# Kernel tuning notes

Hardware: AMD Instinct MI355X
Metric: run time of the kernel (lower is better)

The kernel has to match this reference:

```python
import jax, jax.numpy as jnp
import numpy as np

LN_EPS = 1e-5


def _layernorm(h, gamma, beta):
    mu = jnp.mean(h, axis=-1, keepdims=True)
    var = jnp.mean(jnp.square(h - mu), axis=-1, keepdims=True)
    return (h - mu) * jax.lax.rsqrt(var + LN_EPS) * gamma + beta


def setup_inputs() -> dict:
    key = jax.random.key(0)
    ks = jax.random.split(key, 8)
    B, D, d_model, vocab = 8, 14, 256, 1024
    n_leaf = 2 ** D
    leaf_ids = jax.random.randint(ks[0], (B, n_leaf), 0, vocab)
    op_ids = jax.random.randint(ks[1], (B, n_leaf - 1), 0, vocab)  # heap/BFS order
    tok_emb = jax.random.normal(ks[2], (vocab, d_model), jnp.float32)
    dep_emb = jax.random.normal(ks[3], (15, d_model), jnp.float32)
    idx_emb = jax.random.normal(ks[4], (2, d_model), jnp.float32)
    W = jax.random.normal(ks[5], (7 * d_model, d_model), jnp.float32) / np.sqrt(7 * d_model)
    b = jnp.zeros((d_model,), jnp.float32)
    gamma = jnp.ones((d_model,), jnp.float32)
    beta = jnp.zeros((d_model,), jnp.float32)
    return {"leaf_ids": leaf_ids, "op_ids": op_ids, "tok_emb": tok_emb,
            "dep_emb": dep_emb, "idx_emb": idx_emb, "W": W, "b": b,
            "gamma": gamma, "beta": beta}


def reference(leaf_ids, op_ids, tok_emb, dep_emb, idx_emb, W, b, gamma, beta):
    B, n_leaf = leaf_ids.shape
    D = int(np.log2(n_leaf))  # leaf depth
    d_model = tok_emb.shape[1]
    # leaves: token embedding + depth embedding (OpCombiner path for non-Op nodes)
    emb = tok_emb[leaf_ids] + dep_emb[D]                       # [B, 2^D, dm]
    # process internal levels bottom-up (fixed-size loop over tree depth)
    for d in reversed(range(D)):
        n = 2 ** d
        nid = op_ids[:, n - 1:2 * n - 1]                       # [B, n]
        left, right = emb[:, 0::2], emb[:, 1::2]              # children depth d+1
        e_op = tok_emb[nid]                                    # [B, n, dm]
        dvec = jnp.broadcast_to(dep_emb[d + 1], (B, n, d_model))
        il = jnp.broadcast_to(idx_emb[0], (B, n, d_model))
        ir = jnp.broadcast_to(idx_emb[1], (B, n, d_model))
        x = jnp.concatenate([e_op, left, right, dvec, il, dvec, ir], axis=-1)  # [B,n,7dm]
        h = jax.nn.relu(jnp.einsum('bnk,kd->bnd', x, W) + b)
        emb = _layernorm(h, gamma, beta)
    return emb[:, 0]                                           # root embedding [B, dm]
```

## Files before the change

### kernel.cpp

```cpp
#include <hip/hip_runtime.h>

typedef float f32x4 __attribute__((ext_vector_type(4)));
typedef short bf16x8 __attribute__((ext_vector_type(8)));

__device__ inline unsigned short f2bf(float f) {
    unsigned int u = __builtin_bit_cast(unsigned int, f);
    unsigned int r = (u + 0x7FFFu + ((u >> 16) & 1u)) >> 16;
    return (unsigned short)r;
}
__device__ inline float bf2f(unsigned short u) {
    unsigned int x = ((unsigned int)u) << 16;
    return __builtin_bit_cast(float, x);
}
__device__ inline float f4get(const float4& v, int e) {
    return e == 0 ? v.x : (e == 1 ? v.y : (e == 2 ? v.z : v.w));
}

__global__ __launch_bounds__(256) void k_prep(const float* __restrict__ tok,
                                              const float* __restrict__ W,
                                              const float* __restrict__ dep,
                                              const float* __restrict__ idx,
                                              const float* __restrict__ bvec,
                                              unsigned short* __restrict__ tokbf,
                                              unsigned short* __restrict__ WTbf,
                                              float* __restrict__ carrp) {
    __shared__ float s_tile[64][65];
    int bx = blockIdx.x;
    if (bx < 256) {
        int i = bx * 256 + threadIdx.x;
        const float4 v = *(const float4*)(tok + (long)i * 4);
        ushort4 o;
        o.x = f2bf(v.x); o.y = f2bf(v.y); o.z = f2bf(v.z); o.w = f2bf(v.w);
        *(ushort4*)(tokbf + (long)i * 4) = o;
    } else if (bx < 304) {
        int bb = bx - 256;
        int sec = bb >> 4;
        int tt = bb & 15;
        int k0 = (tt >> 2) * 64, j0 = (tt & 3) * 64;
        int tx = threadIdx.x & 63, ty = threadIdx.x >> 6;
#pragma unroll
        for (int r = 0; r < 16; r++) {
            int kk = ty * 16 + r;
            s_tile[kk][tx] = W[(sec * 256 + k0 + kk) * 256 + j0 + tx];
        }
        __syncthreads();
#pragma unroll
        for (int r = 0; r < 16; r++) {
            int jj = ty * 16 + r;
            WTbf[(sec * 256 + j0 + jj) * 256 + k0 + tx] = f2bf(s_tile[tx][jj]);
        }
    } else {
        int q = bx - 304;
        int d = q >> 3;
        int c = q & 7;
        int j = threadIdx.x;
        float acc = (c == 0) ? bvec[j] : 0.f;
        int kbeg = c * 32, kend = kbeg + 32;
#pragma unroll 4
        for (int k = kbeg; k < kend; k++) {
            float dv = dep[(d + 1) * 256 + k];
            acc += dv * (W[(768 + k) * 256 + j] + W[(1280 + k) * 256 + j]);
            acc += idx[k] * W[(1024 + k) * 256 + j];
            acc += idx[256 + k] * W[(1536 + k) * 256 + j];
        }
        if (d == 13) {
#pragma unroll 4
            for (int k = kbeg; k < kend; k++) {
                float dv = dep[14 * 256 + k];
                acc += dv * (W[(256 + k) * 256 + j] + W[(512 + k) * 256 + j]);
            }
        }
        carrp[(long)q * 256 + j] = acc;
    }
}

__global__ __launch_bounds__(256) void k_carrsum(const float* __restrict__ carrp,
                                                 float* __restrict__ carr) {
    int d = blockIdx.x;
    int j = threadIdx.x;
    float s = 0.f;
#pragma unroll
    for (int c = 0; c < 8; c++) s += carrp[(long)(d * 8 + c) * 256 + j];
    carr[d * 256 + j] = s;
}

__global__ __launch_bounds__(256) void k_ttmm(const unsigned short* __restrict__ tokbf,
                                              const unsigned short* __restrict__ WTbf,
                                              unsigned short* __restrict__ T) {
    int wid = threadIdx.x >> 6, lane = threadIdx.x & 63;
    int l15 = lane & 15, l4 = lane >> 4;
    int row0 = blockIdx.x * 32;
    int sec = blockIdx.y;

    f32x4 acc[2][4] = {};
    for (int kk = 0; kk < 8; kk++) {
        int k0 = kk * 32 + l4 * 8;
        bf16x8 af[2], bfr[4];
#pragma unroll
        for (int mi = 0; mi < 2; mi++)
            af[mi] = *(const bf16x8*)(tokbf + (long)(row0 + mi * 16 + l15) * 256 + k0);
#pragma unroll
        for (int ni = 0; ni < 4; ni++)
            bfr[ni] = *(const bf16x8*)(WTbf + (long)(sec * 256 + wid * 64 + ni * 16 + l15) * 256 + k0);
#pragma unroll
        for (int mi = 0; mi < 2; mi++)
#pragma unroll
            for (int ni = 0; ni < 4; ni++)
                acc[mi][ni] = __builtin_amdgcn_mfma_f32_16x16x32_bf16(af[mi], bfr[ni],
                                                                     acc[mi][ni], 0, 0, 0);
    }
#pragma unroll
    for (int mi = 0; mi < 2; mi++)
#pragma unroll
        for (int r = 0; r < 4; r++) {
            int row = row0 + mi * 16 + l4 * 4 + r;
#pragma unroll
            for (int ni = 0; ni < 4; ni++) {
                int c = wid * 64 + ni * 16 + l15;
                T[(long)sec * 262144 + (long)row * 256 + c] = f2bf(acc[mi][ni][r]);
            }
        }
}

__global__ __launch_bounds__(256) void k_level12f(const int* __restrict__ leaf_ids,
                                                  const int* __restrict__ op_ids,
                                                  const unsigned short* __restrict__ T,
                                                  const float* __restrict__ carr,
                                                  const float* __restrict__ gamma,
                                                  const float* __restrict__ beta,
                                                  const unsigned short* __restrict__ WTbf,
                                                  unsigned short* __restrict__ ebuf_out) {
    __shared__ unsigned short sA[64 * 256];
    __shared__ int s_nid13[64];
    __shared__ int s_leaf[128];
    __shared__ int s_nid[32];
    __shared__ float s_part[4][32][2];
    int b = blockIdx.y;
    int row0 = blockIdx.x * 32;
    int t = threadIdx.x;
    int wid = t >> 6, lane = t & 63;
    int l15 = lane & 15, l4 = lane >> 4;
    const unsigned short* T0 = T;
    const unsigned short* T1 = T + 262144;
    const unsigned short* T2 = T + 524288;

    if (t < 64) s_nid13[t] = op_ids[b * 16383 + 8191 + 2 * row0 + t];
    if (t < 128) s_leaf[t] = leaf_ids[b * 16384 + 4 * row0 + t];
    if (t < 32) s_nid[t] = op_ids[b * 16383 + 4095 + row0 + t];
    __syncthreads();

    {
        const float* c13 = carr + 13 * 256;
        float4 dd[4], g4[4], b4[4];
#pragma unroll
        for (int q = 0; q < 4; q++) {
            int c0 = l15 * 16 + q * 4;
            dd[q] = *(const float4*)(c13 + c0);
            g4[q] = *(const float4*)(gamma + c0);
            b4[q] = *(const float4*)(beta + c0);
        }
#pragma unroll
        for (int j = 0; j < 4; j++) {
            int node = wid * 16 + j * 4 + l4;
            int nid = s_nid13[node];
            int ll = s_leaf[2 * node], lr = s_leaf[2 * node + 1];
            bf16x8 a0 = *(const bf16x8*)(T0 + (long)nid * 256 + l15 * 16);
            bf16x8 a1 = *(const bf16x8*)(T0 + (long)nid * 256 + l15 * 16 + 8);
            bf16x8 b0 = *(const bf16x8*)(T1 + (long)ll * 256 + l15 * 16);
            bf16x8 b1 = *(const bf16x8*)(T1 + (long)ll * 256 + l15 * 16 + 8);
            bf16x8 c0 = *(const bf16x8*)(T2 + (long)lr * 256 + l15 * 16);
            bf16x8 c1 = *(const bf16x8*)(T2 + (long)lr * 256 + l15 * 16 + 8);
            float v[16];
            float s = 0.f, s2 = 0.f;
#pragma unroll
            for (int e = 0; e < 8; e++) {
                float x = bf2f((unsigned short)a0[e]) + bf2f((unsigned short)b0[e]) +
                          bf2f((unsigned short)c0[e]) + f4get(dd[e >> 2], e & 3);
                x = fmaxf(x, 0.f);
                v[e] = x;
                s += x;
                s2 += x * x;
            }
#pragma unroll
            for (int e = 0; e < 8; e++) {
                float x = bf2f((unsigned short)a1[e]) + bf2f((unsigned short)b1[e]) +
                          bf2f((unsigned short)c1[e]) + f4get(dd[2 + (e >> 2)], e & 3);
                x = fmaxf(x, 0.f);
                v[8 + e] = x;
                s += x;
                s2 += x * x;
            }
#pragma unroll
            for (int m = 1; m < 16; m <<= 1) {
                s += __shfl_xor(s, m);
                s2 += __shfl_xor(s2, m);
            }
            float mu = s * (1.f / 256.f);
            float rs = rsqrtf(s2 * (1.f / 256.f) - mu * mu + 1e-5f);
            int swz = ((node >> 1) & 7) << 4;
            bf16x8 o0, o1;
#pragma unroll
            for (int e = 0; e < 8; e++) {
                o0[e] = (short)f2bf((v[e] - mu) * rs * f4get(g4[e >> 2], e & 3) +
                                    f4get(b4[e >> 2], e & 3));
                o1[e] = (short)f2bf((v[8 + e] - mu) * rs * f4get(g4[2 + (e >> 2)], e & 3) +
                                    f4get(b4[2 + (e >> 2)], e & 3));
            }
            *(bf16x8*)((char*)sA + node * 512 + ((l15 * 32) ^ swz)) = o0;
            *(bf16x8*)((char*)sA + node * 512 + ((l15 * 32 + 16) ^ swz)) = o1;
        }
    }
    __syncthreads();

    f32x4 acc[2][4] = {};
    for (int kk = 0; kk < 16; kk++) {
        int k0 = kk * 32 + l4 * 8;
        int hi = k0 >> 8;
        int binr = (k0 & 255) * 2;
        bf16x8 af[2], bfr[4];
#pragma unroll
        for (int mi = 0; mi < 2; mi++) {
            int node = 2 * (mi * 16 + l15) + hi;
            af[mi] = *(const bf16x8*)((const char*)sA + node * 512 + (binr ^ (((node >> 1) & 7) << 4)));
        }
        const unsigned short* Wb = WTbf + (long)(256 + hi * 256) * 256;
        int innerk = k0 & 255;
#pragma unroll
        for (int ni = 0; ni < 4; ni++) {
            int cn = wid * 64 + ni * 16 + l15;
            bfr[ni] = *(const bf16x8*)(Wb + (long)cn * 256 + innerk);
        }
#pragma unroll
        for (int mi = 0; mi < 2; mi++)
#pragma unroll
            for (int ni = 0; ni < 4; ni++)
                acc[mi][ni] = __builtin_amdgcn_mfma_f32_16x16x32_bf16(af[mi], bfr[ni],
                                                                     acc[mi][ni], 0, 0, 0);
    }

    const float* carr_d = carr + 12 * 256;
    float cv[4], gv[4], bv[4];
#pragma unroll
    for (int ni = 0; ni < 4; ni++) {
        int c = wid * 64 + ni * 16 + l15;
        cv[ni] = carr_d[c];
        gv[ni] = gamma[c];
        bv[ni] = beta[c];
    }

#pragma unroll
    for (int mi = 0; mi < 2; mi++) {
#pragma unroll
        for (int r = 0; r < 4; r++) {
            int row = mi * 16 + l4 * 4 + r;
            int nid = s_nid[row];
            float s = 0.f, s2 = 0.f;
#pragma unroll
            for (int ni = 0; ni < 4; ni++) {
                int c = wid * 64 + ni * 16 + l15;
                float h = acc[mi][ni][r] + bf2f(T0[(long)nid * 256 + c]) + cv[ni];
                h = fmaxf(h, 0.f);
                acc[mi][ni][r] = h;
                s += h;
                s2 += h * h;
            }
#pragma unroll
            for (int m = 1; m < 16; m <<= 1) {
                s += __shfl_xor(s, m);
                s2 += __shfl_xor(s2, m);
            }
            if (l15 == 0) {
                s_part[wid][row][0] = s;
                s_part[wid][row][1] = s2;
            }
        }
    }
    __syncthreads();

#pragma unroll
    for (int mi = 0; mi < 2; mi++) {
#pragma unroll
        for (int r = 0; r < 4; r++) {
            int row = mi * 16 + l4 * 4 + r;
            float s = s_part[0][row][0] + s_part[1][row][0] + s_part[2][row][0] + s_part[3][row][0];
            float s2 = s_part[0][row][1] + s_part[1][row][1] + s_part[2][row][1] + s_part[3][row][1];
            float mu = s * (1.f / 256.f);
            float rs = rsqrtf(s2 * (1.f / 256.f) - mu * mu + 1e-5f);
            unsigned short* o = ebuf_out + ((long)b * 4096 + row0 + row) * 256;
#pragma unroll
            for (int ni = 0; ni < 4; ni++) {
                int c = wid * 64 + ni * 16 + l15;
                o[c] = f2bf((acc[mi][ni][r] - mu) * rs * gv[ni] + bv[ni]);
            }
        }
    }
}

__global__ __attribute__((amdgpu_waves_per_eu(2, 2))) __launch_bounds__(512)
void k_mid(const unsigned short* __restrict__ prev,
           unsigned short* __restrict__ outbuf,
           const int* __restrict__ op_ids,
           const unsigned short* __restrict__ T0,
           const float* __restrict__ carr,
           const float* __restrict__ gamma,
           const float* __restrict__ beta,
           const unsigned short* __restrict__ WTbf) {
    __shared__ unsigned short sA[64 * 256];
    __shared__ unsigned short sB[64 * 256];
    __shared__ float s_part[8][64][2];
    int b = blockIdx.x >> 5;
    int q = blockIdx.x & 31;
    int t = threadIdx.x;
    int wid = t >> 6, lane = t & 63;
    int l15 = lane & 15, l4 = lane >> 4;

    bf16x8 breg[16][2];
#pragma unroll
    for (int kk = 0; kk < 16; kk++) {
        int k0 = kk * 32 + l4 * 8;
        int hi = k0 >> 8;
        int innerk = k0 & 255;
        const unsigned short* Wb = WTbf + (long)(256 + hi * 256) * 256;
#pragma unroll
        for (int ni = 0; ni < 2; ni++) {
            int cn = wid * 32 + ni * 16 + l15;
            breg[kk][ni] = *(const bf16x8*)(Wb + (long)cn * 256 + innerk);
        }
    }

    float gv[2], bv[2];
#pragma unroll
    for (int ni = 0; ni < 2; ni++) {
        int c = wid * 32 + ni * 16 + l15;
        gv[ni] = gamma[c];
        bv[ni] = beta[c];
    }

    unsigned short* cur = sA;
    unsigned short* nxt = sB;

    for (int ld = 11; ld >= 8; ld--) {
        int ng = 1 << ld;
        int m = ng >> 5;
        int mtiles = (m + 15) >> 4;

        float tv[4][4][2];
#pragma unroll
        for (int mi = 0; mi < 4; mi++)
            if (mi < mtiles)
#pragma unroll
                for (int r = 0; r < 4; r++) {
                    int row = mi * 16 + l4 * 4 + r;
                    int rc = row < m ? row : m - 1;
                    int nid = op_ids[b * 16383 + (ng - 1) + q * m + rc];
#pragma unroll
                    for (int ni = 0; ni < 2; ni++)
                        tv[mi][r][ni] = bf2f(T0[(long)nid * 256 + wid * 32 + ni * 16 + l15]);
                }

        f32x4 acc[4][2] = {};
        if (ld == 11) {
            const unsigned short* X = prev + ((long)b * 4096 + q * 128) * 256;
#pragma unroll
            for (int kk = 0; kk < 16; kk++) {
                int k0 = kk * 32 + l4 * 8;
                bf16x8 af[4];
#pragma unroll
                for (int mi = 0; mi < 4; mi++)
                    af[mi] = *(const bf16x8*)(X + (long)(mi * 16 + l15) * 512 + k0);
#pragma unroll
                for (int mi = 0; mi < 4; mi++)
#pragma unroll
                    for (int ni = 0; ni < 2; ni++)
                        acc[mi][ni] = __builtin_amdgcn_mfma_f32_16x16x32_bf16(af[mi], breg[kk][ni],
                                                                             acc[mi][ni], 0, 0, 0);
            }
        } else {
#pragma unroll
            for (int kk = 0; kk < 16; kk++) {
                int k0 = kk * 32 + l4 * 8;
                int hi = k0 >> 8;
                int binr = (k0 & 255) * 2;
                bf16x8 af[4];
#pragma unroll
                for (int mi = 0; mi < 4; mi++)
                    if (mi < mtiles) {
                        int node = 2 * (mi * 16 + l15) + hi;
                        af[mi] = *(const bf16x8*)((const char*)cur + node * 512 +
                                                  (binr ^ (((node >> 1) & 7) << 4)));
                    }
#pragma unroll
                for (int mi = 0; mi < 4; mi++)
                    if (mi < mtiles)
#pragma unroll
                        for (int ni = 0; ni < 2; ni++)
                            acc[mi][ni] = __builtin_amdgcn_mfma_f32_16x16x32_bf16(
                                af[mi], breg[kk][ni], acc[mi][ni], 0, 0, 0);
            }
        }

        const float* carr_d = carr + ld * 256;
        float cv[2];
#pragma unroll
        for (int ni = 0; ni < 2; ni++) cv[ni] = carr_d[wid * 32 + ni * 16 + l15];

#pragma unroll
        for (int mi = 0; mi < 4; mi++)
            if (mi < mtiles)
#pragma unroll
                for (int r = 0; r < 4; r++) {
                    float s = 0.f, s2 = 0.f;
#pragma unroll
                    for (int ni = 0; ni < 2; ni++) {
                        float hh = fmaxf(acc[mi][ni][r] + tv[mi][r][ni] + cv[ni], 0.f);
                        acc[mi][ni][r] = hh;
                        s += hh;
                        s2 += hh * hh;
                    }
#pragma unroll
                    for (int m2 = 1; m2 < 16; m2 <<= 1) {
                        s += __shfl_xor(s, m2);
                        s2 += __shfl_xor(s2, m2);
                    }
                    if (l15 == 0) {
                        int row = mi * 16 + l4 * 4 + r;
                        s_part[wid][row][0] = s;
                        s_part[wid][row][1] = s2;
                    }
                }
        __syncthreads();

#pragma unroll
        for (int mi = 0; mi < 4; mi++)
            if (mi < mtiles)
#pragma unroll
                for (int r = 0; r < 4; r++) {
                    int row = mi * 16 + l4 * 4 + r;
                    if (row < m) {
                        float s = 0.f, s2 = 0.f;
#pragma unroll
                        for (int w = 0; w < 8; w++) {
                            s += s_part[w][row][0];
                            s2 += s_part[w][row][1];
                        }
                        float mu = s * (1.f / 256.f);
                        float rs = rsqrtf(s2 * (1.f / 256.f) - mu * mu + 1e-5f);
#pragma unroll
                        for (int ni = 0; ni < 2; ni++) {
                            int c = wid * 32 + ni * 16 + l15;
                            float val = (acc[mi][ni][r] - mu) * rs * gv[ni] + bv[ni];
                            if (ld == 8) {
                                outbuf[((long)b * 256 + q * 8 + row) * 256 + c] = f2bf(val);
                            } else {
                                *(unsigned short*)((char*)nxt + row * 512 +
                                                   ((c * 2) ^ (((row >> 1) & 7) << 4))) = f2bf(val);
                            }
                        }
                    }
                }
        __syncthreads();
        unsigned short* tmp = cur;
        cur = nxt;
        nxt = tmp;
    }
}

__global__ __attribute__((amdgpu_waves_per_eu(2, 2))) __launch_bounds__(512)
void k_tail(const unsigned short* __restrict__ prev,
            const int* __restrict__ op_ids,
            const unsigned short* __restrict__ T0,
            const float* __restrict__ carr,
            const float* __restrict__ gamma,
            const float* __restrict__ beta,
            const unsigned short* __restrict__ WTbf,
            unsigned short* __restrict__ mid) {
    __shared__ unsigned short sA[32 * 256];
    __shared__ unsigned short sB[32 * 256];
    __shared__ int s_nid_all[255];
    __shared__ float s_part[8][16][2];
    int b = blockIdx.x >> 3;
    int q = blockIdx.x & 7;
    int t = threadIdx.x;
    int wid = t >> 6, lane = t & 63;
    int l15 = lane & 15, l4 = lane >> 4;

    bf16x8 breg[16][2];
#pragma unroll
    for (int kk = 0; kk < 16; kk++) {
        int k0 = kk * 32 + l4 * 8;
        int hi = k0 >> 8;
        int innerk = k0 & 255;
        const unsigned short* Wb = WTbf + (long)(256 + hi * 256) * 256;
#pragma unroll
        for (int ni = 0; ni < 2; ni++) {
            int cn = wid * 32 + ni * 16 + l15;
            breg[kk][ni] = *(const bf16x8*)(Wb + (long)cn * 256 + innerk);
        }
    }

    if (t < 255) s_nid_all[t] = op_ids[b * 16383 + t];
    float gv[2], bv[2];
#pragma unroll
    for (int ni = 0; ni < 2; ni++) {
        int c = wid * 32 + ni * 16 + l15;
        gv[ni] = gamma[c];
        bv[ni] = beta[c];
    }
    __syncthreads();

    unsigned short* cur = sA;
    unsigned short* nxt = sB;

    for (int ld = 7; ld >= 3; ld--) {
        int ng = 1 << ld;
        int m = ng >> 3;

        float tv[4][2];
#pragma unroll
        for (int r = 0; r < 4; r++) {
            int row = l4 * 4 + r;
            int rc = row < m ? row : m - 1;
            int nid = s_nid_all[(ng - 1) + q * m + rc];
#pragma unroll
            for (int ni = 0; ni < 2; ni++)
                tv[r][ni] = bf2f(T0[(long)nid * 256 + wid * 32 + ni * 16 + l15]);
        }

        f32x4 acc[2] = {};
        if (ld == 7) {
            const unsigned short* X = prev + ((long)b * 256 + q * 32) * 256;
#pragma unroll
            for (int kk = 0; kk < 16; kk++) {
                int k0 = kk * 32 + l4 * 8;
                bf16x8 af = *(const bf16x8*)(X + (long)l15 * 512 + k0);
#pragma unroll
                for (int ni = 0; ni < 2; ni++)
                    acc[ni] = __builtin_amdgcn_mfma_f32_16x16x32_bf16(af, breg[kk][ni], acc[ni],
                                                                      0, 0, 0);
            }
        } else {
#pragma unroll
            for (int kk = 0; kk < 16; kk++) {
                int k0 = kk * 32 + l4 * 8;
                int hi = k0 >> 8;
                int binr = (k0 & 255) * 2;
                int node = 2 * l15 + hi;
                bf16x8 af = *(const bf16x8*)((const char*)cur + node * 512 +
                                             (binr ^ (((node >> 1) & 7) << 4)));
#pragma unroll
                for (int ni = 0; ni < 2; ni++)
                    acc[ni] = __builtin_amdgcn_mfma_f32_16x16x32_bf16(af, breg[kk][ni], acc[ni],
                                                                      0, 0, 0);
            }
        }

        const float* carr_d = carr + ld * 256;
        float cv[2];
#pragma unroll
        for (int ni = 0; ni < 2; ni++) cv[ni] = carr_d[wid * 32 + ni * 16 + l15];

#pragma unroll
        for (int r = 0; r < 4; r++) {
            float s = 0.f, s2 = 0.f;
#pragma unroll
            for (int ni = 0; ni < 2; ni++) {
                float hh = fmaxf(acc[ni][r] + tv[r][ni] + cv[ni], 0.f);
                acc[ni][r] = hh;
                s += hh;
                s2 += hh * hh;
            }
#pragma unroll
            for (int m2 = 1; m2 < 16; m2 <<= 1) {
                s += __shfl_xor(s, m2);
                s2 += __shfl_xor(s2, m2);
            }
            if (l15 == 0) {
                int row = l4 * 4 + r;
                s_part[wid][row][0] = s;
                s_part[wid][row][1] = s2;
            }
        }
        __syncthreads();

#pragma unroll
        for (int r = 0; r < 4; r++) {
            int row = l4 * 4 + r;
            if (row < m) {
                float s = 0.f, s2 = 0.f;
#pragma unroll
                for (int w = 0; w < 8; w++) {
                    s += s_part[w][row][0];
                    s2 += s_part[w][row][1];
                }
                float mu = s * (1.f / 256.f);
                float rs = rsqrtf(s2 * (1.f / 256.f) - mu * mu + 1e-5f);
#pragma unroll
                for (int ni = 0; ni < 2; ni++) {
                    int c = wid * 32 + ni * 16 + l15;
                    float val = (acc[ni][r] - mu) * rs * gv[ni] + bv[ni];
                    if (ld == 3) {
                        mid[(long)(b * 8 + q) * 256 + c] = f2bf(val);
                    } else {
                        *(unsigned short*)((char*)nxt + row * 512 +
                                           ((c * 2) ^ (((row >> 1) & 7) << 4))) = f2bf(val);
                    }
                }
            }
        }
        __syncthreads();
        unsigned short* tmp = cur;
        cur = nxt;
        nxt = tmp;
    }
}

__global__ __launch_bounds__(256) void k_root2(const unsigned short* __restrict__ mid,
                                               const int* __restrict__ op_ids,
                                               const unsigned short* __restrict__ T0,
                                               const float* __restrict__ carr,
                                               const float* __restrict__ gamma,
                                               const float* __restrict__ beta,
                                               const unsigned short* __restrict__ WTbf,
                                               float* __restrict__ out) {
    __shared__ unsigned short sL2[32 * 256];
    __shared__ unsigned short sL1[16 * 256];
    __shared__ float s_part[4][32][2];
    __shared__ int s_n2[32], s_n1[16], s_n0[8];
    int t = threadIdx.x;
    int wid = t >> 6, lane = t & 63;
    int l15 = lane & 15, l4 = lane >> 4;

    if (t < 32) s_n2[t] = op_ids[(t >> 2) * 16383 + 3 + (t & 3)];
    if (t < 16) s_n1[t] = op_ids[(t >> 1) * 16383 + 1 + (t & 1)];
    if (t < 8) s_n0[t] = op_ids[t * 16383];
    float gv[4], bv[4];
#pragma unroll
    for (int ni = 0; ni < 4; ni++) {
        int c = wid * 64 + ni * 16 + l15;
        gv[ni] = gamma[c];
        bv[ni] = beta[c];
    }
    __syncthreads();

    {
        f32x4 acc[2][4] = {};
        for (int kk = 0; kk < 16; kk++) {
            int k0 = kk * 32 + l4 * 8;
            int hi = k0 >> 8;
            int innerk = k0 & 255;
            bf16x8 af[2], bfr[4];
#pragma unroll
            for (int mi = 0; mi < 2; mi++)
                af[mi] = *(const bf16x8*)(mid + (long)(mi * 16 + l15) * 512 + k0);
            const unsigned short* Wb = WTbf + (long)(256 + hi * 256) * 256;
#pragma unroll
            for (int ni = 0; ni < 4; ni++) {
                int cn = wid * 64 + ni * 16 + l15;
                bfr[ni] = *(const bf16x8*)(Wb + (long)cn * 256 + innerk);
            }
#pragma unroll
            for (int mi = 0; mi < 2; mi++)
#pragma unroll
                for (int ni = 0; ni < 4; ni++)
                    acc[mi][ni] = __builtin_amdgcn_mfma_f32_16x16x32_bf16(af[mi], bfr[ni],
                                                                         acc[mi][ni], 0, 0, 0);
        }
        const float* carr2 = carr + 2 * 256;
        float cv[4];
#pragma unroll
        for (int ni = 0; ni < 4; ni++) cv[ni] = carr2[wid * 64 + ni * 16 + l15];
#pragma unroll
        for (int mi = 0; mi < 2; mi++)
#pragma unroll
            for (int r = 0; r < 4; r++) {
                int row = mi * 16 + l4 * 4 + r;
                int nid = s_n2[row];
                float s = 0.f, s2 = 0.f;
#pragma unroll
                for (int ni = 0; ni < 4; ni++) {
                    int c = wid * 64 + ni * 16 + l15;
                    float h = fmaxf(acc[mi][ni][r] + bf2f(T0[(long)nid * 256 + c]) + cv[ni], 0.f);
                    acc[mi][ni][r] = h;
                    s += h;
                    s2 += h * h;
                }
#pragma unroll
                for (int m = 1; m < 16; m <<= 1) {
                    s += __shfl_xor(s, m);
                    s2 += __shfl_xor(s2, m);
                }
                if (l15 == 0) {
                    s_part[wid][row][0] = s;
                    s_part[wid][row][1] = s2;
                }
            }
        __syncthreads();
#pragma unroll
        for (int mi = 0; mi < 2; mi++)
#pragma unroll
            for (int r = 0; r < 4; r++) {
                int row = mi * 16 + l4 * 4 + r;
                float s = s_part[0][row][0] + s_part[1][row][0] + s_part[2][row][0] + s_part[3][row][0];
                float s2 = s_part[0][row][1] + s_part[1][row][1] + s_part[2][row][1] + s_part[3][row][1];
                float mu = s * (1.f / 256.f);
                float rs = rsqrtf(s2 * (1.f / 256.f) - mu * mu + 1e-5f);
#pragma unroll
                for (int ni = 0; ni < 4; ni++) {
                    int c = wid * 64 + ni * 16 + l15;
                    *(unsigned short*)((char*)sL2 + row * 512 +
                                       ((c * 2) ^ (((row >> 1) & 7) << 4))) =
                        f2bf((acc[mi][ni][r] - mu) * rs * gv[ni] + bv[ni]);
                }
            }
        __syncthreads();
    }

    {
        f32x4 acc[4] = {};
        for (int kk = 0; kk < 16; kk++) {
            int k0 = kk * 32 + l4 * 8;
            int hi = k0 >> 8;
            int innerk = k0 & 255;
            int binr = (k0 & 255) * 2;
            int node = 2 * l15 + hi;
            bf16x8 af = *(const bf16x8*)((const char*)sL2 + node * 512 +
                                         (binr ^ (((node >> 1) & 7) << 4)));
            const unsigned short* Wb = WTbf + (long)(256 + hi * 256) * 256;
#pragma unroll
            for (int ni = 0; ni < 4; ni++) {
                int cn = wid * 64 + ni * 16 + l15;
                bf16x8 bfr = *(const bf16x8*)(Wb + (long)cn * 256 + innerk);
                acc[ni] = __builtin_amdgcn_mfma_f32_16x16x32_bf16(af, bfr, acc[ni], 0, 0, 0);
            }
        }
        const float* carr1 = carr + 256;
        float cv[4];
#pragma unroll
        for (int ni = 0; ni < 4; ni++) cv[ni] = carr1[wid * 64 + ni * 16 + l15];
#pragma unroll
        for (int r = 0; r < 4; r++) {
            int row = l4 * 4 + r;
            int nid = s_n1[row];
            float s = 0.f, s2 = 0.f;
#pragma unroll
            for (int ni = 0; ni < 4; ni++) {
                int c = wid * 64 + ni * 16 + l15;
                float h = fmaxf(acc[ni][r] + bf2f(T0[(long)nid * 256 + c]) + cv[ni], 0.f);
                acc[ni][r] = h;
                s += h;
                s2 += h * h;
            }
#pragma unroll
            for (int m = 1; m < 16; m <<= 1) {
                s += __shfl_xor(s, m);
                s2 += __shfl_xor(s2, m);
            }
            if (l15 == 0) {
                s_part[wid][row][0] = s;
                s_part[wid][row][1] = s2;
            }
        }
        __syncthreads();
#pragma unroll
        for (int r = 0; r < 4; r++) {
            int row = l4 * 4 + r;
            float s = s_part[0][row][0] + s_part[1][row][0] + s_part[2][row][0] + s_part[3][row][0];
            float s2 = s_part[0][row][1] + s_part[1][row][1] + s_part[2][row][1] + s_part[3][row][1];
            float mu = s * (1.f / 256.f);
            float rs = rsqrtf(s2 * (1.f / 256.f) - mu * mu + 1e-5f);
#pragma unroll
            for (int ni = 0; ni < 4; ni++) {
                int c = wid * 64 + ni * 16 + l15;
                *(unsigned short*)((char*)sL1 + row * 512 +
                                   ((c * 2) ^ (((row >> 1) & 7) << 4))) =
                    f2bf((acc[ni][r] - mu) * rs * gv[ni] + bv[ni]);
            }
        }
        __syncthreads();
    }

    {
        f32x4 acc[4] = {};
        for (int kk = 0; kk < 16; kk++) {
            int k0 = kk * 32 + l4 * 8;
            int hi = k0 >> 8;
            int innerk = k0 & 255;
            int binr = (k0 & 255) * 2;
            int node = 2 * (l15 & 7) + hi;
            bf16x8 af = *(const bf16x8*)((const char*)sL1 + node * 512 +
                                         (binr ^ (((node >> 1) & 7) << 4)));
            const unsigned short* Wb = WTbf + (long)(256 + hi * 256) * 256;
#pragma unroll
            for (int ni = 0; ni < 4; ni++) {
                int cn = wid * 64 + ni * 16 + l15;
                bf16x8 bfr = *(const bf16x8*)(Wb + (long)cn * 256 + innerk);
                acc[ni] = __builtin_amdgcn_mfma_f32_16x16x32_bf16(af, bfr, acc[ni], 0, 0, 0);
            }
        }
        float cv[4];
#pragma unroll
        for (int ni = 0; ni < 4; ni++) cv[ni] = carr[wid * 64 + ni * 16 + l15];
#pragma unroll
        for (int r = 0; r < 4; r++) {
            int row = l4 * 4 + r;
            int nid = s_n0[row & 7];
            float s = 0.f, s2 = 0.f;
#pragma unroll
            for (int ni = 0; ni < 4; ni++) {
                int c = wid * 64 + ni * 16 + l15;
                float h = fmaxf(acc[ni][r] + bf2f(T0[(long)nid * 256 + c]) + cv[ni], 0.f);
                acc[ni][r] = h;
                s += h;
                s2 += h * h;
            }
#pragma unroll
            for (int m = 1; m < 16; m <<= 1) {
                s += __shfl_xor(s, m);
                s2 += __shfl_xor(s2, m);
            }
            if (l15 == 0) {
                s_part[wid][row][0] = s;
                s_part[wid][row][1] = s2;
            }
        }
        __syncthreads();
#pragma unroll
        for (int r = 0; r < 4; r++) {
            int row = l4 * 4 + r;
            if (row < 8) {
                float s = s_part[0][row][0] + s_part[1][row][0] + s_part[2][row][0] + s_part[3][row][0];
                float s2 = s_part[0][row][1] + s_part[1][row][1] + s_part[2][row][1] + s_part[3][row][1];
                float mu = s * (1.f / 256.f);
                float rs = rsqrtf(s2 * (1.f / 256.f) - mu * mu + 1e-5f);
#pragma unroll
                for (int ni = 0; ni < 4; ni++) {
                    int c = wid * 64 + ni * 16 + l15;
                    out[row * 256 + c] = (acc[ni][r] - mu) * rs * gv[ni] + bv[ni];
                }
            }
        }
    }
}

extern "C" void kernel_launch(void* const* d_in, const int* in_sizes, int n_in,
                              void* d_out, int out_size, void* d_ws, size_t ws_size,
                              hipStream_t stream) {
    const int* leaf_ids = (const int*)d_in[0];
    const int* op_ids = (const int*)d_in[1];
    const float* tok = (const float*)d_in[2];
    const float* dep = (const float*)d_in[3];
    const float* idx = (const float*)d_in[4];
    const float* W = (const float*)d_in[5];
    const float* bvec = (const float*)d_in[6];
    const float* gamma = (const float*)d_in[7];
    const float* beta = (const float*)d_in[8];
    float* out = (float*)d_out;

    char* ws = (char*)d_ws;
    unsigned short* T = (unsigned short*)(ws);
    unsigned short* WTbf = (unsigned short*)(ws + 3u * 1024 * 1024);
    unsigned short* tokbf = (unsigned short*)(ws + 3u * 1024 * 1024 + 512 * 1024);
    float* carr = (float*)(ws + 4u * 1024 * 1024 + 64 * 1024);
    float* carrp = (float*)(ws + 5u * 1024 * 1024);
    unsigned short* mid = (unsigned short*)(ws + 6u * 1024 * 1024);
    unsigned short* ebufA = (unsigned short*)(ws + 8u * 1024 * 1024);
    unsigned short* ebufB = (unsigned short*)(ws + 40u * 1024 * 1024);

    k_prep<<<416, 256, 0, stream>>>(tok, W, dep, idx, bvec, tokbf, WTbf, carrp);
    k_carrsum<<<14, 256, 0, stream>>>(carrp, carr);
    k_ttmm<<<dim3(32, 3), 256, 0, stream>>>(tokbf, WTbf, T);

    k_level12f<<<dim3(128, 8), 256, 0, stream>>>(leaf_ids, op_ids, T, carr, gamma, beta, WTbf,
                                                 ebufA);
    k_mid<<<256, 512, 0, stream>>>(ebufA, ebufB, op_ids, T, carr, gamma, beta, WTbf);
    k_tail<<<64, 512, 0, stream>>>(ebufB, op_ids, T, carr, gamma, beta, WTbf, mid);
    k_root2<<<1, 256, 0, stream>>>(mid, op_ids, T, carr, gamma, beta, WTbf, out);
}
```

Baseline: 183.2 us.

## Fuse level-13/12 kernel into mid-level kernel keeping level-12 output in LDS

Merges the separate level-13/12 kernel into the mid-level kernel. Each 512-thread block now computes its 128 level-12 nodes in two halves and writes them to shared memory instead of a global buffer, then continues straight into levels 11..8. This removes a kernel launch and the global write and read-back of the level-12 embeddings (about 16 MB bf16). In exchange, the level-13/12 work runs on only 256 blocks with two waves per EU instead of 1024 smaller blocks, which reduces parallelism for the gather-heavy phase. The fused kernel also uses twice the LDS of the old mid kernel.

```diff
diff --git a/kernel.cpp b/kernel.cpp
--- a/kernel.cpp
+++ b/kernel.cpp
@@ -122,21 +122,22 @@
         }
 }
 
-__global__ __launch_bounds__(256) void k_level12f(const int* __restrict__ leaf_ids,
-                                                  const int* __restrict__ op_ids,
-                                                  const unsigned short* __restrict__ T,
-                                                  const float* __restrict__ carr,
-                                                  const float* __restrict__ gamma,
-                                                  const float* __restrict__ beta,
-                                                  const unsigned short* __restrict__ WTbf,
-                                                  unsigned short* __restrict__ ebuf_out) {
-    __shared__ unsigned short sA[64 * 256];
-    __shared__ int s_nid13[64];
-    __shared__ int s_leaf[128];
-    __shared__ int s_nid[32];
-    __shared__ float s_part[4][32][2];
-    int b = blockIdx.y;
-    int row0 = blockIdx.x * 32;
+__global__ __attribute__((amdgpu_waves_per_eu(2, 2))) __launch_bounds__(512)
+void k_big(const int* __restrict__ leaf_ids,
+           const int* __restrict__ op_ids,
+           const unsigned short* __restrict__ T,
+           const float* __restrict__ carr,
+           const float* __restrict__ gamma,
+           const float* __restrict__ beta,
+           const unsigned short* __restrict__ WTbf,
+           unsigned short* __restrict__ outbuf) {
+    __shared__ unsigned short sA[128 * 256];
+    __shared__ unsigned short sB[128 * 256];
+    __shared__ int s_nid13[128];
+    __shared__ int s_leaf[256];
+    __shared__ float s_part[8][64][2];
+    int b = blockIdx.x >> 5;
+    int q = blockIdx.x & 31;
     int t = threadIdx.x;
     int wid = t >> 6, lane = t & 63;
     int l15 = lane & 15, l4 = lane >> 4;
@@ -144,176 +145,6 @@
     const unsigned short* T1 = T + 262144;
     const unsigned short* T2 = T + 524288;
 
-    if (t < 64) s_nid13[t] = op_ids[b * 16383 + 8191 + 2 * row0 + t];
-    if (t < 128) s_leaf[t] = leaf_ids[b * 16384 + 4 * row0 + t];
-    if (t < 32) s_nid[t] = op_ids[b * 16383 + 4095 + row0 + t];
-    __syncthreads();
-
-    {
-        const float* c13 = carr + 13 * 256;
-        float4 dd[4], g4[4], b4[4];
-#pragma unroll
-        for (int q = 0; q < 4; q++) {
-            int c0 = l15 * 16 + q * 4;
-            dd[q] = *(const float4*)(c13 + c0);
-            g4[q] = *(const float4*)(gamma + c0);
-            b4[q] = *(const float4*)(beta + c0);
-        }
-#pragma unroll
-        for (int j = 0; j < 4; j++) {
-            int node = wid * 16 + j * 4 + l4;
-            int nid = s_nid13[node];
-            int ll = s_leaf[2 * node], lr = s_leaf[2 * node + 1];
-            bf16x8 a0 = *(const bf16x8*)(T0 + (long)nid * 256 + l15 * 16);
-            bf16x8 a1 = *(const bf16x8*)(T0 + (long)nid * 256 + l15 * 16 + 8);
-            bf16x8 b0 = *(const bf16x8*)(T1 + (long)ll * 256 + l15 * 16);
-            bf16x8 b1 = *(const bf16x8*)(T1 + (long)ll * 256 + l15 * 16 + 8);
-            bf16x8 c0 = *(const bf16x8*)(T2 + (long)lr * 256 + l15 * 16);
-            bf16x8 c1 = *(const bf16x8*)(T2 + (long)lr * 256 + l15 * 16 + 8);
-            float v[16];
-            float s = 0.f, s2 = 0.f;
-#pragma unroll
-            for (int e = 0; e < 8; e++) {
-                float x = bf2f((unsigned short)a0[e]) + bf2f((unsigned short)b0[e]) +
-                          bf2f((unsigned short)c0[e]) + f4get(dd[e >> 2], e & 3);
-                x = fmaxf(x, 0.f);
-                v[e] = x;
-                s += x;
-                s2 += x * x;
-            }
-#pragma unroll
-            for (int e = 0; e < 8; e++) {
-                float x = bf2f((unsigned short)a1[e]) + bf2f((unsigned short)b1[e]) +
-                          bf2f((unsigned short)c1[e]) + f4get(dd[2 + (e >> 2)], e & 3);
-                x = fmaxf(x, 0.f);
-                v[8 + e] = x;
-                s += x;
-                s2 += x * x;
-            }
-#pragma unroll
-            for (int m = 1; m < 16; m <<= 1) {
-                s += __shfl_xor(s, m);
-                s2 += __shfl_xor(s2, m);
-            }
-            float mu = s * (1.f / 256.f);
-            float rs = rsqrtf(s2 * (1.f / 256.f) - mu * mu + 1e-5f);
-            int swz = ((node >> 1) & 7) << 4;
-            bf16x8 o0, o1;
-#pragma unroll
-            for (int e = 0; e < 8; e++) {
-                o0[e] = (short)f2bf((v[e] - mu) * rs * f4get(g4[e >> 2], e & 3) +
-                                    f4get(b4[e >> 2], e & 3));
-                o1[e] = (short)f2bf((v[8 + e] - mu) * rs * f4get(g4[2 + (e >> 2)], e & 3) +
-                                    f4get(b4[2 + (e >> 2)], e & 3));
-            }
-            *(bf16x8*)((char*)sA + node * 512 + ((l15 * 32) ^ swz)) = o0;
-            *(bf16x8*)((char*)sA + node * 512 + ((l15 * 32 + 16) ^ swz)) = o1;
-        }
-    }
-    __syncthreads();
-
-    f32x4 acc[2][4] = {};
-    for (int kk = 0; kk < 16; kk++) {
-        int k0 = kk * 32 + l4 * 8;
-        int hi = k0 >> 8;
-        int binr = (k0 & 255) * 2;
-        bf16x8 af[2], bfr[4];
-#pragma unroll
-        for (int mi = 0; mi < 2; mi++) {
-            int node = 2 * (mi * 16 + l15) + hi;
-            af[mi] = *(const bf16x8*)((const char*)sA + node * 512 + (binr ^ (((node >> 1) & 7) << 4)));
-        }
-        const unsigned short* Wb = WTbf + (long)(256 + hi * 256) * 256;
-        int innerk = k0 & 255;
-#pragma unroll
-        for (int ni = 0; ni < 4; ni++) {
-            int cn = wid * 64 + ni * 16 + l15;
-            bfr[ni] = *(const bf16x8*)(Wb + (long)cn * 256 + innerk);
-        }
-#pragma unroll
-        for (int mi = 0; mi < 2; mi++)
-#pragma unroll
-            for (int ni = 0; ni < 4; ni++)
-                acc[mi][ni] = __builtin_amdgcn_mfma_f32_16x16x32_bf16(af[mi], bfr[ni],
-                                                                     acc[mi][ni], 0, 0, 0);
-    }
-
-    const float* carr_d = carr + 12 * 256;
-    float cv[4], gv[4], bv[4];
-#pragma unroll
-    for (int ni = 0; ni < 4; ni++) {
-        int c = wid * 64 + ni * 16 + l15;
-        cv[ni] = carr_d[c];
-        gv[ni] = gamma[c];
-        bv[ni] = beta[c];
-    }
-
-#pragma unroll
-    for (int mi = 0; mi < 2; mi++) {
-#pragma unroll
-        for (int r = 0; r < 4; r++) {
-            int row = mi * 16 + l4 * 4 + r;
-            int nid = s_nid[row];
-            float s = 0.f, s2 = 0.f;
-#pragma unroll
-            for (int ni = 0; ni < 4; ni++) {
-                int c = wid * 64 + ni * 16 + l15;
-                float h = acc[mi][ni][r] + bf2f(T0[(long)nid * 256 + c]) + cv[ni];
-                h = fmaxf(h, 0.f);
-                acc[mi][ni][r] = h;
-                s += h;
-                s2 += h * h;
-            }
-#pragma unroll
-            for (int m = 1; m < 16; m <<= 1) {
-                s += __shfl_xor(s, m);
-                s2 += __shfl_xor(s2, m);
-            }
-            if (l15 == 0) {
-                s_part[wid][row][0] = s;
-                s_part[wid][row][1] = s2;
-            }
-        }
-    }
-    __syncthreads();
-
-#pragma unroll
-    for (int mi = 0; mi < 2; mi++) {
-#pragma unroll
-        for (int r = 0; r < 4; r++) {
-            int row = mi * 16 + l4 * 4 + r;
-            float s = s_part[0][row][0] + s_part[1][row][0] + s_part[2][row][0] + s_part[3][row][0];
-            float s2 = s_part[0][row][1] + s_part[1][row][1] + s_part[2][row][1] + s_part[3][row][1];
-            float mu = s * (1.f / 256.f);
-            float rs = rsqrtf(s2 * (1.f / 256.f) - mu * mu + 1e-5f);
-            unsigned short* o = ebuf_out + ((long)b * 4096 + row0 + row) * 256;
-#pragma unroll
-            for (int ni = 0; ni < 4; ni++) {
-                int c = wid * 64 + ni * 16 + l15;
-                o[c] = f2bf((acc[mi][ni][r] - mu) * rs * gv[ni] + bv[ni]);
-            }
-        }
-    }
-}
-
-__global__ __attribute__((amdgpu_waves_per_eu(2, 2))) __launch_bounds__(512)
-void k_mid(const unsigned short* __restrict__ prev,
-           unsigned short* __restrict__ outbuf,
-           const int* __restrict__ op_ids,
-           const unsigned short* __restrict__ T0,
-           const float* __restrict__ carr,
-           const float* __restrict__ gamma,
-           const float* __restrict__ beta,
-           const unsigned short* __restrict__ WTbf) {
-    __shared__ unsigned short sA[64 * 256];
-    __shared__ unsigned short sB[64 * 256];
-    __shared__ float s_part[8][64][2];
-    int b = blockIdx.x >> 5;
-    int q = blockIdx.x & 31;
-    int t = threadIdx.x;
-    int wid = t >> 6, lane = t & 63;
-    int l15 = lane & 15, l4 = lane >> 4;
-
     bf16x8 breg[16][2];
 #pragma unroll
     for (int kk = 0; kk < 16; kk++) {
@@ -336,9 +167,165 @@
         bv[ni] = beta[c];
     }
 
-    unsigned short* cur = sA;
-    unsigned short* nxt = sB;
-
+#pragma unroll 1
+    for (int h = 0; h < 2; h++) {
+        if (t < 128) s_nid13[t] = op_ids[b * 16383 + 8191 + q * 256 + h * 128 + t];
+        if (t < 256) s_leaf[t] = leaf_ids[b * 16384 + q * 512 + h * 256 + t];
+        __syncthreads();
+
+        {
+            const float* c13 = carr + 13 * 256;
+            float4 dd[4], g4[4], b4[4];
+#pragma unroll
+            for (int q2 = 0; q2 < 4; q2++) {
+                int c0 = l15 * 16 + q2 * 4;
+                dd[q2] = *(const float4*)(c13 + c0);
+                g4[q2] = *(const float4*)(gamma + c0);
+                b4[q2] = *(const float4*)(beta + c0);
+            }
+#pragma unroll
+            for (int j = 0; j < 4; j++) {
+                int node = wid * 16 + j * 4 + l4;
+                int nid = s_nid13[node];
+                int ll = s_leaf[2 * node], lr = s_leaf[2 * node + 1];
+                bf16x8 a0 = *(const bf16x8*)(T0 + (long)nid * 256 + l15 * 16);
+                bf16x8 a1 = *(const bf16x8*)(T0 + (long)nid * 256 + l15 * 16 + 8);
+                bf16x8 b0 = *(const bf16x8*)(T1 + (long)ll * 256 + l15 * 16);
+                bf16x8 b1 = *(const bf16x8*)(T1 + (long)ll * 256 + l15 * 16 + 8);
+                bf16x8 c0 = *(const bf16x8*)(T2 + (long)lr * 256 + l15 * 16);
+                bf16x8 c1 = *(const bf16x8*)(T2 + (long)lr * 256 + l15 * 16 + 8);
+                float v[16];
+                float s = 0.f, s2 = 0.f;
+#pragma unroll
+                for (int e = 0; e < 8; e++) {
+                    float x = bf2f((unsigned short)a0[e]) + bf2f((unsigned short)b0[e]) +
+                              bf2f((unsigned short)c0[e]) + f4get(dd[e >> 2], e & 3);
+                    x = fmaxf(x, 0.f);
+                    v[e] = x;
+                    s += x;
+                    s2 += x * x;
+                }
+#pragma unroll
+                for (int e = 0; e < 8; e++) {
+                    float x = bf2f((unsigned short)a1[e]) + bf2f((unsigned short)b1[e]) +
+                              bf2f((unsigned short)c1[e]) + f4get(dd[2 + (e >> 2)], e & 3);
+                    x = fmaxf(x, 0.f);
+                    v[8 + e] = x;
+                    s += x;
+                    s2 += x * x;
+                }
+#pragma unroll
+                for (int m = 1; m < 16; m <<= 1) {
+                    s += __shfl_xor(s, m);
+                    s2 += __shfl_xor(s2, m);
+                }
+                float mu = s * (1.f / 256.f);
+                float rs = rsqrtf(s2 * (1.f / 256.f) - mu * mu + 1e-5f);
+                int swz = ((node >> 1) & 7) << 4;
+                bf16x8 o0, o1;
+#pragma unroll
+                for (int e = 0; e < 8; e++) {
+                    o0[e] = (short)f2bf((v[e] - mu) * rs * f4get(g4[e >> 2], e & 3) +
+                                        f4get(b4[e >> 2], e & 3));
+                    o1[e] = (short)f2bf((v[8 + e] - mu) * rs * f4get(g4[2 + (e >> 2)], e & 3) +
+                                        f4get(b4[2 + (e >> 2)], e & 3));
+                }
+                *(bf16x8*)((char*)sA + node * 512 + ((l15 * 32) ^ swz)) = o0;
+                *(bf16x8*)((char*)sA + node * 512 + ((l15 * 32 + 16) ^ swz)) = o1;
+            }
+        }
+        __syncthreads();
+
+        float tv[4][4][2];
+#pragma unroll
+        for (int mi = 0; mi < 4; mi++)
+#pragma unroll
+            for (int r = 0; r < 4; r++) {
+                int row = mi * 16 + l4 * 4 + r;
+                int nid = op_ids[b * 16383 + 4095 + q * 128 + h * 64 + row];
+#pragma unroll
+                for (int ni = 0; ni < 2; ni++)
+                    tv[mi][r][ni] = bf2f(T0[(long)nid * 256 + wid * 32 + ni * 16 + l15]);
+            }
+
+        f32x4 acc[4][2] = {};
+#pragma unroll
+        for (int kk = 0; kk < 16; kk++) {
+            int k0 = kk * 32 + l4 * 8;
+            int hi = k0 >> 8;
+            int binr = (k0 & 255) * 2;
+            bf16x8 af[4];
+#pragma unroll
+            for (int mi = 0; mi < 4; mi++) {
+                int node = 2 * (mi * 16 + l15) + hi;
+                af[mi] = *(const bf16x8*)((const char*)sA + node * 512 +
+                                          (binr ^ (((node >> 1) & 7) << 4)));
+            }
+#pragma unroll
+            for (int mi = 0; mi < 4; mi++)
+#pragma unroll
+                for (int ni = 0; ni < 2; ni++)
+                    acc[mi][ni] = __builtin_amdgcn_mfma_f32_16x16x32_bf16(af[mi], breg[kk][ni],
+                                                                         acc[mi][ni], 0, 0, 0);
+        }
+
+        const float* carr12 = carr + 12 * 256;
+        float cv[2];
+#pragma unroll
+        for (int ni = 0; ni < 2; ni++) cv[ni] = carr12[wid * 32 + ni * 16 + l15];
+
+#pragma unroll
+        for (int mi = 0; mi < 4; mi++)
+#pragma unroll
+            for (int r = 0; r < 4; r++) {
+                float s = 0.f, s2 = 0.f;
+#pragma unroll
+                for (int ni = 0; ni < 2; ni++) {
+                    float hh = fmaxf(acc[mi][ni][r] + tv[mi][r][ni] + cv[ni], 0.f);
+                    acc[mi][ni][r] = hh;
+                    s += hh;
+                    s2 += hh * hh;
+                }
+#pragma unroll
+                for (int m2 = 1; m2 < 16; m2 <<= 1) {
+                    s += __shfl_xor(s, m2);
+                    s2 += __shfl_xor(s2, m2);
+                }
+                if (l15 == 0) {
+                    int row = mi * 16 + l4 * 4 + r;
+                    s_part[wid][row][0] = s;
+                    s_part[wid][row][1] = s2;
+                }
+            }
+        __syncthreads();
+
+#pragma unroll
+        for (int mi = 0; mi < 4; mi++)
+#pragma unroll
+            for (int r = 0; r < 4; r++) {
+                int row = mi * 16 + l4 * 4 + r;
+                float s = 0.f, s2 = 0.f;
+#pragma unroll
+                for (int w = 0; w < 8; w++) {
+                    s += s_part[w][row][0];
+                    s2 += s_part[w][row][1];
+                }
+                float mu = s * (1.f / 256.f);
+                float rs = rsqrtf(s2 * (1.f / 256.f) - mu * mu + 1e-5f);
+                int hrow = h * 64 + row;
+#pragma unroll
+                for (int ni = 0; ni < 2; ni++) {
+                    int c = wid * 32 + ni * 16 + l15;
+                    *(unsigned short*)((char*)sB + hrow * 512 +
+                                       ((c * 2) ^ (((hrow >> 1) & 7) << 4))) =
+                        f2bf((acc[mi][ni][r] - mu) * rs * gv[ni] + bv[ni]);
+                }
+            }
+        __syncthreads();
+    }
+
+    unsigned short* cur = sB;
+    unsigned short* nxt = sA;
     for (int ld = 11; ld >= 8; ld--) {
         int ng = 1 << ld;
         int m = ng >> 5;
@@ -359,44 +346,26 @@
                 }
 
         f32x4 acc[4][2] = {};
-        if (ld == 11) {
-            const unsigned short* X = prev + ((long)b * 4096 + q * 128) * 256;
-#pragma unroll
-            for (int kk = 0; kk < 16; kk++) {
-                int k0 = kk * 32 + l4 * 8;
-                bf16x8 af[4];
-#pragma unroll
-                for (int mi = 0; mi < 4; mi++)
-                    af[mi] = *(const bf16x8*)(X + (long)(mi * 16 + l15) * 512 + k0);
-#pragma unroll
-                for (int mi = 0; mi < 4; mi++)
+#pragma unroll
+        for (int kk = 0; kk < 16; kk++) {
+            int k0 = kk * 32 + l4 * 8;
+            int hi = k0 >> 8;
+            int binr = (k0 & 255) * 2;
+            bf16x8 af[4];
+#pragma unroll
+            for (int mi = 0; mi < 4; mi++)
+                if (mi < mtiles) {
+                    int node = 2 * (mi * 16 + l15) + hi;
+                    af[mi] = *(const bf16x8*)((const char*)cur + node * 512 +
+                                              (binr ^ (((node >> 1) & 7) << 4)));
+                }
+#pragma unroll
+            for (int mi = 0; mi < 4; mi++)
+                if (mi < mtiles)
 #pragma unroll
                     for (int ni = 0; ni < 2; ni++)
-                        acc[mi][ni] = __builtin_amdgcn_mfma_f32_16x16x32_bf16(af[mi], breg[kk][ni],
-                                                                             acc[mi][ni], 0, 0, 0);
-            }
-        } else {
-#pragma unroll
-            for (int kk = 0; kk < 16; kk++) {
-                int k0 = kk * 32 + l4 * 8;
-                int hi = k0 >> 8;
-                int binr = (k0 & 255) * 2;
-                bf16x8 af[4];
-#pragma unroll
-                for (int mi = 0; mi < 4; mi++)
-                    if (mi < mtiles) {
-                        int node = 2 * (mi * 16 + l15) + hi;
-                        af[mi] = *(const bf16x8*)((const char*)cur + node * 512 +
-                                                  (binr ^ (((node >> 1) & 7) << 4)));
-                    }
-#pragma unroll
-                for (int mi = 0; mi < 4; mi++)
-                    if (mi < mtiles)
-#pragma unroll
-                        for (int ni = 0; ni < 2; ni++)
-                            acc[mi][ni] = __builtin_amdgcn_mfma_f32_16x16x32_bf16(
-                                af[mi], breg[kk][ni], acc[mi][ni], 0, 0, 0);
-            }
+                        acc[mi][ni] = __builtin_amdgcn_mfma_f32_16x16x32_bf16(
+                            af[mi], breg[kk][ni], acc[mi][ni], 0, 0, 0);
         }
 
         const float* carr_d = carr + ld * 256;
@@ -863,16 +832,13 @@
     float* carr = (float*)(ws + 4u * 1024 * 1024 + 64 * 1024);
     float* carrp = (float*)(ws + 5u * 1024 * 1024);
     unsigned short* mid = (unsigned short*)(ws + 6u * 1024 * 1024);
-    unsigned short* ebufA = (unsigned short*)(ws + 8u * 1024 * 1024);
-    unsigned short* ebufB = (unsigned short*)(ws + 40u * 1024 * 1024);
+    unsigned short* ebufB = (unsigned short*)(ws + 8u * 1024 * 1024);
 
     k_prep<<<416, 256, 0, stream>>>(tok, W, dep, idx, bvec, tokbf, WTbf, carrp);
     k_carrsum<<<14, 256, 0, stream>>>(carrp, carr);
     k_ttmm<<<dim3(32, 3), 256, 0, stream>>>(tokbf, WTbf, T);
 
-    k_level12f<<<dim3(128, 8), 256, 0, stream>>>(leaf_ids, op_ids, T, carr, gamma, beta, WTbf,
-                                                 ebufA);
-    k_mid<<<256, 512, 0, stream>>>(ebufA, ebufB, op_ids, T, carr, gamma, beta, WTbf);
+    k_big<<<256, 512, 0, stream>>>(leaf_ids, op_ids, T, carr, gamma, beta, WTbf, ebufB);
     k_tail<<<64, 512, 0, stream>>>(ebufB, op_ids, T, carr, gamma, beta, WTbf, mid);
     k_root2<<<1, 256, 0, stream>>>(mid, op_ids, T, carr, gamma, beta, WTbf, out);
 }
```

New measurement: 186.6 us. Within noise of the previous version (+1.8%).
